# Kernel tuning notes

Hardware: AMD Instinct MI355X
Metric: run time of the kernel (lower is better)

The kernel has to match this reference:

```python
import jax, jax.numpy as jnp
import numpy as np

B, L, D = 1, 2048, 3072
NH, HD = 24, 128
MLP = 12288  # 4*D


def setup_inputs() -> dict:
    key = jax.random.key(0)
    ks = jax.random.split(key, 12)
    s = 0.02
    return {
        "scratchA": jnp.zeros((B, L, D + MLP), jnp.float32),
        "x": jax.random.normal(ks[0], (B, L, D), jnp.float32),
        "vec": jax.random.normal(ks[1], (B, D), jnp.float32),
        "pe": jax.random.normal(ks[2], (1, 1, L, HD // 2, 2, 2), jnp.float32),
        # Modulation: Linear(D, 3*D), stored as [in, out]
        "mod_w": jax.random.normal(ks[3], (D, 3 * D), jnp.float32) * s,
        "mod_b": jnp.zeros((3 * D,), jnp.float32),
        # linear1: Linear(D, 3*D + MLP)
        "w1": jax.random.normal(ks[4], (D, 3 * D + MLP), jnp.float32) * s,
        "b1": jnp.zeros((3 * D + MLP,), jnp.float32),
        # linear2: Linear(D + MLP, D)
        "w2": jax.random.normal(ks[5], (D + MLP, D), jnp.float32) * s,
        "b2": jnp.zeros((D,), jnp.float32),
        # QKNorm RMSNorm scales over head_dim
        "q_scale": jnp.ones((HD,), jnp.float32),
        "k_scale": jnp.ones((HD,), jnp.float32),
    }


def _rms_norm(t, scale, eps=1e-6):
    n = jax.lax.rsqrt(jnp.mean(t * t, axis=-1, keepdims=True) + eps)
    return t * (n * scale)


def _layer_norm(t, eps=1e-6):
    mu = jnp.mean(t, axis=-1, keepdims=True)
    var = jnp.mean(jnp.square(t - mu), axis=-1, keepdims=True)
    return (t - mu) * jax.lax.rsqrt(var + eps)


def _apply_rope(t, pe):
    # t: [B, NH, L, HD]; pe: [1, 1, L, HD//2, 2, 2]
    b, h, l, d = t.shape
    tr = t.reshape(b, h, l, d // 2, 1, 2)
    out = pe[..., 0] * tr[..., 0] + pe[..., 1] * tr[..., 1]  # [B,NH,L,HD//2,2]
    return out.reshape(b, h, l, d)


def reference(scratchA, x, vec, pe, mod_w, mod_b, w1, b1, w2, b2, q_scale, k_scale):
    # Modulation: silu + linear + chunk(3)
    mod = (jnp.dot(jax.nn.silu(vec), mod_w) + mod_b)[:, None, :]  # [B,1,3D]
    mod_shift, mod_scale, mod_gate = jnp.split(mod, 3, axis=-1)

    # adaLN modulation of pre-norm
    x_mod = mod_shift + (1.0 + mod_scale) * _layer_norm(x)

    # fused linear1 -> qkv + mlp
    h = jnp.dot(x_mod, w1) + b1  # [B, L, 3D + MLP]
    qkv, mlp = h[..., : 3 * D], h[..., 3 * D :]
    qkv = qkv.reshape(B, L, 3, NH, HD).transpose(2, 0, 3, 1, 4)  # [3,B,NH,L,HD]
    q, k, v = qkv[0], qkv[1], qkv[2]

    # QK RMSNorm
    q = _rms_norm(q, q_scale)
    k = _rms_norm(k, k_scale)

    # RoPE
    q = _apply_rope(q, pe)
    k = _apply_rope(k, pe)

    # scaled dot-product attention
    scale = HD ** -0.5
    scores = jnp.einsum("bhqd,bhkd->bhqk", q, k) * scale
    probs = jax.nn.softmax(scores, axis=-1)
    attn = jnp.einsum("bhqk,bhkd->bhqd", probs, v)  # [B,NH,L,HD]
    attn = attn.transpose(0, 2, 1, 3).reshape(B, L, D)

    # scratch buffer = [attention out | gelu(mlp)] (scratchA is just a buffer)
    scratch = jnp.concatenate([attn, jax.nn.gelu(mlp, approximate=True)], axis=-1)

    out = jnp.dot(scratch, w2) + b2
    return x + mod_gate * out
```

## Files before the change

kernel.cpp:

```cpp
#include <hip/hip_runtime.h>

typedef unsigned short u16;
typedef __bf16 bf16x8 __attribute__((ext_vector_type(8)));
typedef float f32x4 __attribute__((ext_vector_type(4)));

#define L_    2048
#define D_    3072
#define NH_   24
#define HD_   128
#define MLP_  12288
#define HCOLS 21504
#define SCOLS 15360

__device__ __forceinline__ float bf2f(u16 u) { return __uint_as_float(((unsigned)u) << 16); }
__device__ __forceinline__ u16 f2bf(float f) {
    unsigned b = __float_as_uint(f);
    b += 0x7FFF + ((b >> 16) & 1);
    return (u16)(b >> 16);
}
__device__ __forceinline__ void gld_lds16(const u16* g, u16* l) {
    __builtin_amdgcn_global_load_lds((const __attribute__((address_space(1))) void*)g,
                                     (__attribute__((address_space(3))) void*)l, 16, 0, 0);
}

template <int BM, int BN>
__global__ __launch_bounds__(256) void gemm_bt(
    const u16* __restrict__ A, const u16* __restrict__ Bt,
    const float* __restrict__ bias, void* __restrict__ Cv,
    int M, int N, int K, int ldC,
    long long sA, long long sB, long long sC,
    float alpha, int outBf16)
{
    constexpr int BK = 32;
    __shared__ __align__(16) u16 As[BM * BK];
    __shared__ __align__(16) u16 Bs[BN * BK];
    const int t = threadIdx.x, w = t >> 6, lane = t & 63;
    const int quad = lane >> 4, r16 = lane & 15;
    const int m0 = blockIdx.y * BM, n0 = blockIdx.x * BN;
    const u16* Ab = A + (size_t)blockIdx.z * sA;
    const u16* Bb = Bt + (size_t)blockIdx.z * sB;
    constexpr int WM = BM / 2, WN = BN / 2, TI = WM / 16, TJ = WN / 16;
    const int wm = (w >> 1) * WM, wn = (w & 1) * WN;

    f32x4 acc[TI][TJ];
#pragma unroll
    for (int i = 0; i < TI; ++i)
#pragma unroll
        for (int j = 0; j < TJ; ++j) acc[i][j] = (f32x4){0.f, 0.f, 0.f, 0.f};

    constexpr int AR = (BM * BK * 2) / 4096;
    constexpr int BR = (BN * BK * 2) / 4096;

    for (int k0 = 0; k0 < K; k0 += BK) {
#pragma unroll
        for (int r = 0; r < AR; ++r) {
            int o = r * 4096 + w * 1024 + lane * 16;
            int row = o >> 6, cb = o & 63;
            gld_lds16(Ab + (size_t)(m0 + row) * K + k0 + (cb >> 1), As + (o >> 1));
        }
#pragma unroll
        for (int r = 0; r < BR; ++r) {
            int o = r * 4096 + w * 1024 + lane * 16;
            int row = o >> 6, cb = o & 63;
            gld_lds16(Bb + (size_t)(n0 + row) * K + k0 + (cb >> 1), Bs + (o >> 1));
        }
        __syncthreads();
        bf16x8 af[TI], bfr[TJ];
#pragma unroll
        for (int i = 0; i < TI; ++i)
            af[i] = *(const bf16x8*)&As[(wm + i * 16 + r16) * BK + quad * 8];
#pragma unroll
        for (int j = 0; j < TJ; ++j)
            bfr[j] = *(const bf16x8*)&Bs[(wn + j * 16 + r16) * BK + quad * 8];
#pragma unroll
        for (int i = 0; i < TI; ++i)
#pragma unroll
            for (int j = 0; j < TJ; ++j)
                acc[i][j] = __builtin_amdgcn_mfma_f32_16x16x32_bf16(af[i], bfr[j], acc[i][j], 0, 0, 0);
        __syncthreads();
    }

    if (outBf16) {
        u16* Cb = (u16*)Cv + (size_t)blockIdx.z * sC;
#pragma unroll
        for (int i = 0; i < TI; ++i)
#pragma unroll
            for (int rr = 0; rr < 4; ++rr) {
                int m = m0 + wm + i * 16 + quad * 4 + rr;
                u16* crow = Cb + (size_t)m * ldC;
#pragma unroll
                for (int j = 0; j < TJ; ++j) {
                    int n = n0 + wn + j * 16 + r16;
                    float v = acc[i][j][rr] * alpha;
                    if (bias) v += bias[n];
                    crow[n] = f2bf(v);
                }
            }
    } else {
        float* Cb = (float*)Cv + (size_t)blockIdx.z * sC;
#pragma unroll
        for (int i = 0; i < TI; ++i)
#pragma unroll
            for (int rr = 0; rr < 4; ++rr) {
                int m = m0 + wm + i * 16 + quad * 4 + rr;
                float* crow = Cb + (size_t)m * ldC;
#pragma unroll
                for (int j = 0; j < TJ; ++j) {
                    int n = n0 + wn + j * 16 + r16;
                    float v = acc[i][j][rr] * alpha;
                    if (bias) v += bias[n];
                    crow[n] = v;
                }
            }
    }
}

__global__ __launch_bounds__(256) void transpose_to_bf16(
    const float* __restrict__ in, u16* __restrict__ out, int R, int C)
{
    __shared__ float tile[32][33];
    int c0 = blockIdx.x * 32, r0 = blockIdx.y * 32;
    int tx = threadIdx.x & 31, ty = threadIdx.x >> 5;
#pragma unroll
    for (int i = 0; i < 32; i += 8)
        tile[ty + i][tx] = in[(size_t)(r0 + ty + i) * C + c0 + tx];
    __syncthreads();
#pragma unroll
    for (int i = 0; i < 32; i += 8)
        out[(size_t)(c0 + ty + i) * R + r0 + tx] = f2bf(tile[tx][ty + i]);
}

__global__ void mod_init(const float* __restrict__ mod_b, const float* __restrict__ vec,
                         float* __restrict__ MOD, float* __restrict__ SVEC)
{
    int i = blockIdx.x * 256 + threadIdx.x;
    if (i < 3 * D_) MOD[i] = mod_b[i];
    if (i < D_) { float v = vec[i]; SVEC[i] = v / (1.f + __expf(-v)); }
}

__global__ __launch_bounds__(256) void mod_gemv(
    const float* __restrict__ SVEC, const float* __restrict__ mod_w, float* __restrict__ MOD)
{
    int n = blockIdx.x * 256 + threadIdx.x;
    int k0 = blockIdx.y * 128;
    float acc = 0.f;
#pragma unroll 8
    for (int kk = 0; kk < 128; ++kk)
        acc += SVEC[k0 + kk] * mod_w[(size_t)(k0 + kk) * (3 * D_) + n];
    atomicAdd(&MOD[n], acc);
}

__global__ __launch_bounds__(256) void ln_mod_k(
    const float* __restrict__ x, const float* __restrict__ MOD, u16* __restrict__ XMOD)
{
    int l = blockIdx.x, t = threadIdx.x;
    const float4* xr = (const float4*)(x + (size_t)l * D_);
    float4 v[3];
    float s = 0.f, ss = 0.f;
#pragma unroll
    for (int c = 0; c < 3; ++c) {
        v[c] = xr[c * 256 + t];
        s += v[c].x + v[c].y + v[c].z + v[c].w;
        ss += v[c].x * v[c].x + v[c].y * v[c].y + v[c].z * v[c].z + v[c].w * v[c].w;
    }
    __shared__ float rs[4], rss[4];
    float a = s, b = ss;
    for (int off = 32; off; off >>= 1) { a += __shfl_down(a, off); b += __shfl_down(b, off); }
    if ((t & 63) == 0) { rs[t >> 6] = a; rss[t >> 6] = b; }
    __syncthreads();
    float S = rs[0] + rs[1] + rs[2] + rs[3];
    float SS = rss[0] + rss[1] + rss[2] + rss[3];
    float mu = S * (1.f / D_);
    float var = SS * (1.f / D_) - mu * mu;
    float rstd = rsqrtf(var + 1e-6f);
    u16* orow = XMOD + (size_t)l * D_;
#pragma unroll
    for (int c = 0; c < 3; ++c) {
        int d0 = (c * 256 + t) * 4;
        float vals[4] = {v[c].x, v[c].y, v[c].z, v[c].w};
#pragma unroll
        for (int q = 0; q < 4; ++q) {
            int d = d0 + q;
            float o = MOD[d] + (1.f + MOD[D_ + d]) * ((vals[q] - mu) * rstd);
            orow[d] = f2bf(o);
        }
    }
}

__global__ __launch_bounds__(128) void qkv_rope(
    const u16* __restrict__ h, const float* __restrict__ pe,
    const float* __restrict__ qs, const float* __restrict__ ks,
    u16* __restrict__ Q, u16* __restrict__ Kb)
{
    int l = blockIdx.x, nh = blockIdx.y, tt = blockIdx.z;
    int d = threadIdx.x;
    float xv = bf2f(h[(size_t)l * HCOLS + tt * D_ + nh * HD_ + d]);
    __shared__ float red[2];
    __shared__ float ybuf[HD_];
    float sq = xv * xv;
    for (int off = 32; off; off >>= 1) sq += __shfl_down(sq, off);
    if ((d & 63) == 0) red[d >> 6] = sq;
    __syncthreads();
    float tot = red[0] + red[1];
    float rms = rsqrtf(tot * (1.f / HD_) + 1e-6f);
    const float* scale = (tt == 0) ? qs : ks;
    float y = xv * rms * scale[d];
    ybuf[d] = y;
    __syncthreads();
    int p = d >> 1, j = d & 1;
    float e = ybuf[2 * p], o = ybuf[2 * p + 1];
    const float* pb = pe + ((size_t)l * (HD_ / 2) + p) * 4 + j * 2;
    float out = pb[0] * e + pb[1] * o;
    u16* dst = (tt == 0) ? Q : Kb;
    dst[((size_t)nh * L_ + l) * HD_ + d] = f2bf(out);
}

__global__ __launch_bounds__(256) void v_trans(const u16* __restrict__ h, u16* __restrict__ VT)
{
    int lb = blockIdx.x, nh = blockIdx.y;
    __shared__ u16 tile[HD_][65];
    int t = threadIdx.x;
#pragma unroll
    for (int it = 0; it < 32; ++it) {
        int idx = it * 256 + t;
        int d = idx & 127, ll = idx >> 7;
        tile[d][ll] = h[(size_t)(lb * 64 + ll) * HCOLS + 2 * D_ + nh * HD_ + d];
    }
    __syncthreads();
#pragma unroll
    for (int it = 0; it < 32; ++it) {
        int idx = it * 256 + t;
        int ll = idx & 63, d = idx >> 6;
        VT[((size_t)nh * HD_ + d) * L_ + lb * 64 + ll] = tile[d][ll];
    }
}

__global__ __launch_bounds__(256) void gelu_k(const u16* __restrict__ h, u16* __restrict__ S)
{
    int l = blockIdx.y;
    int m = blockIdx.x * 256 + threadIdx.x;
    float v = bf2f(h[(size_t)l * HCOLS + 3 * D_ + m]);
    float c = 0.7978845608028654f * (v + 0.044715f * v * v * v);
    float g = 0.5f * v * (1.f + tanhf(c));
    S[(size_t)l * SCOLS + D_ + m] = f2bf(g);
}

__global__ __launch_bounds__(256) void softmax_k(const float* __restrict__ S, u16* __restrict__ P)
{
    const int t = threadIdx.x;
    const float* sr = S + (size_t)blockIdx.x * L_;
    u16* pr = P + (size_t)blockIdx.x * L_;
    float v[8];
    float mx = -3.4e38f;
#pragma unroll
    for (int c = 0; c < 8; ++c) { v[c] = sr[c * 256 + t]; mx = fmaxf(mx, v[c]); }
    __shared__ float red[4];
    for (int off = 32; off; off >>= 1) mx = fmaxf(mx, __shfl_down(mx, off));
    if ((t & 63) == 0) red[t >> 6] = mx;
    __syncthreads();
    mx = fmaxf(fmaxf(red[0], red[1]), fmaxf(red[2], red[3]));
    float sum = 0.f;
#pragma unroll
    for (int c = 0; c < 8; ++c) { v[c] = __expf(v[c] - mx); sum += v[c]; }
    __syncthreads();
    for (int off = 32; off; off >>= 1) sum += __shfl_down(sum, off);
    if ((t & 63) == 0) red[t >> 6] = sum;
    __syncthreads();
    sum = red[0] + red[1] + red[2] + red[3];
    float inv = 1.f / sum;
#pragma unroll
    for (int c = 0; c < 8; ++c) pr[c * 256 + t] = f2bf(v[c] * inv);
}

__global__ __launch_bounds__(256) void final_k(
    const float* __restrict__ x, const float* __restrict__ MOD,
    const float* __restrict__ G, float* __restrict__ out)
{
    int l = blockIdx.y;
    int d = blockIdx.x * 256 + threadIdx.x;
    size_t i = (size_t)l * D_ + d;
    out[i] = x[i] + MOD[2 * D_ + d] * G[i];
}

#define W1T_OFF   0ull
#define XMOD_OFF  132120576ull
#define W2T_OFF   144703488ull
#define Q_OFF     239075328ull
#define K_OFF     251658240ull
#define VT_OFF    264241152ull
#define SCR_OFF   276824064ull
#define MOD_OFF   339738624ull
#define SVEC_OFF  339775488ull
#define WS_NEED   339787776ull
#define SCORES_OFF 0ull
#define PROBS_OFF  67108864ull
#define G2_OFF     0ull

extern "C" void kernel_launch(void* const* d_in, const int* in_sizes, int n_in,
                              void* d_out, int out_size, void* d_ws, size_t ws_size,
                              hipStream_t stream)
{
    if (ws_size < WS_NEED) return;

    u16* hbuf = (u16*)d_in[0];
    const float* x     = (const float*)d_in[1];
    const float* vec   = (const float*)d_in[2];
    const float* pe    = (const float*)d_in[3];
    const float* mod_w = (const float*)d_in[4];
    const float* mod_b = (const float*)d_in[5];
    const float* w1    = (const float*)d_in[6];
    const float* b1    = (const float*)d_in[7];
    const float* w2    = (const float*)d_in[8];
    const float* b2    = (const float*)d_in[9];
    const float* qs    = (const float*)d_in[10];
    const float* ks    = (const float*)d_in[11];
    float* out = (float*)d_out;

    char* ws = (char*)d_ws;
    u16* W1T   = (u16*)(ws + W1T_OFF);
    u16* XMOD  = (u16*)(ws + XMOD_OFF);
    u16* W2T   = (u16*)(ws + W2T_OFF);
    u16* Qb    = (u16*)(ws + Q_OFF);
    u16* Kb    = (u16*)(ws + K_OFF);
    u16* VT    = (u16*)(ws + VT_OFF);
    u16* SCR   = (u16*)(ws + SCR_OFF);
    float* MOD  = (float*)(ws + MOD_OFF);
    float* SVEC = (float*)(ws + SVEC_OFF);
    float* SCORES = (float*)(ws + SCORES_OFF);
    u16* PROBS    = (u16*)(ws + PROBS_OFF);
    float* G2     = (float*)(ws + G2_OFF);

    transpose_to_bf16<<<dim3(HCOLS / 32, D_ / 32), 256, 0, stream>>>(w1, W1T, D_, HCOLS);
    transpose_to_bf16<<<dim3(D_ / 32, SCOLS / 32), 256, 0, stream>>>(w2, W2T, SCOLS, D_);

    mod_init<<<36, 256, 0, stream>>>(mod_b, vec, MOD, SVEC);
    mod_gemv<<<dim3(36, 24), 256, 0, stream>>>(SVEC, mod_w, MOD);

    ln_mod_k<<<L_, 256, 0, stream>>>(x, MOD, XMOD);

    gemm_bt<128, 128><<<dim3(HCOLS / 128, L_ / 128, 1), 256, 0, stream>>>(
        XMOD, W1T, b1, hbuf, L_, HCOLS, D_, HCOLS, 0, 0, 0, 1.f, 1);

    qkv_rope<<<dim3(L_, NH_, 2), 128, 0, stream>>>(hbuf, pe, qs, ks, Qb, Kb);
    v_trans<<<dim3(L_ / 64, NH_), 256, 0, stream>>>(hbuf, VT);
    gelu_k<<<dim3(MLP_ / 256, L_), 256, 0, stream>>>(hbuf, SCR);

    const float ascale = 0.08838834764831845f;
    for (int g = 0; g < 6; ++g) {
        const long long hoff = (long long)g * 4 * L_ * HD_;
        gemm_bt<128, 128><<<dim3(L_ / 128, L_ / 128, 4), 256, 0, stream>>>(
            Qb + hoff, Kb + hoff, nullptr, SCORES,
            L_, L_, HD_, L_, (long long)L_ * HD_, (long long)L_ * HD_, (long long)L_ * L_,
            ascale, 0);
        softmax_k<<<4 * L_, 256, 0, stream>>>(SCORES, PROBS);
        gemm_bt<64, 64><<<dim3(HD_ / 64, L_ / 64, 4), 256, 0, stream>>>(
            PROBS, VT + hoff, nullptr, SCR + (size_t)g * 4 * HD_,
            L_, HD_, L_, SCOLS, (long long)L_ * L_, (long long)HD_ * L_, HD_,
            1.f, 1);
    }

    gemm_bt<128, 128><<<dim3(D_ / 128, L_ / 128, 1), 256, 0, stream>>>(
        SCR, W2T, b2, G2, L_, D_, SCOLS, D_, 0, 0, 0, 1.f, 0);

    final_k<<<dim3(D_ / 256, L_), 256, 0, stream>>>(x, MOD, G2, out);
}
```

Baseline: 2.003 ms.

## Fuse GELU and residual gating into GEMM epilogues, swizzle LDS, bf16 scores

```diff
diff --git a/kernel.cpp b/kernel.cpp
--- a/kernel.cpp
+++ b/kernel.cpp
@@ -10,6 +10,7 @@
 #define HD_   128
 #define MLP_  12288
 #define HCOLS 21504
+#define QKVW  9216
 #define SCOLS 15360
 
 __device__ __forceinline__ float bf2f(u16 u) { return __uint_as_float(((unsigned)u) << 16); }
@@ -23,93 +24,100 @@
                                      (__attribute__((address_space(3))) void*)l, 16, 0, 0);
 }
 
-template <int BM, int BN>
-__global__ __launch_bounds__(256) void gemm_bt(
+template <int K, int LDC, int EPI>
+__global__ __launch_bounds__(256) void gemm128(
     const u16* __restrict__ A, const u16* __restrict__ Bt,
     const float* __restrict__ bias, void* __restrict__ Cv,
-    int M, int N, int K, int ldC,
-    long long sA, long long sB, long long sC,
-    float alpha, int outBf16)
+    long long sA, long long sB, long long sC, float alpha,
+    const float* __restrict__ resid, const float* __restrict__ gate)
 {
     constexpr int BK = 32;
-    __shared__ __align__(16) u16 As[BM * BK];
-    __shared__ __align__(16) u16 Bs[BN * BK];
+    __shared__ __align__(16) u16 As[128 * BK];
+    __shared__ __align__(16) u16 Bs[128 * BK];
     const int t = threadIdx.x, w = t >> 6, lane = t & 63;
     const int quad = lane >> 4, r16 = lane & 15;
-    const int m0 = blockIdx.y * BM, n0 = blockIdx.x * BN;
+    const int m0 = blockIdx.x * 128;
+    const int n0 = blockIdx.y * 128;
     const u16* Ab = A + (size_t)blockIdx.z * sA;
     const u16* Bb = Bt + (size_t)blockIdx.z * sB;
-    constexpr int WM = BM / 2, WN = BN / 2, TI = WM / 16, TJ = WN / 16;
-    const int wm = (w >> 1) * WM, wn = (w & 1) * WN;
-
-    f32x4 acc[TI][TJ];
-#pragma unroll
-    for (int i = 0; i < TI; ++i)
-#pragma unroll
-        for (int j = 0; j < TJ; ++j) acc[i][j] = (f32x4){0.f, 0.f, 0.f, 0.f};
-
-    constexpr int AR = (BM * BK * 2) / 4096;
-    constexpr int BR = (BN * BK * 2) / 4096;
+    const int wm = (w >> 1) * 64, wn = (w & 1) * 64;
+
+    f32x4 acc[4][4];
+#pragma unroll
+    for (int i = 0; i < 4; ++i)
+#pragma unroll
+        for (int j = 0; j < 4; ++j) acc[i][j] = (f32x4){0.f, 0.f, 0.f, 0.f};
 
     for (int k0 = 0; k0 < K; k0 += BK) {
 #pragma unroll
-        for (int r = 0; r < AR; ++r) {
+        for (int r = 0; r < 2; ++r) {
             int o = r * 4096 + w * 1024 + lane * 16;
-            int row = o >> 6, cb = o & 63;
-            gld_lds16(Ab + (size_t)(m0 + row) * K + k0 + (cb >> 1), As + (o >> 1));
-        }
-#pragma unroll
-        for (int r = 0; r < BR; ++r) {
+            int row = o >> 6, c = (o >> 4) & 3;
+            int gc = c ^ ((row >> 1) & 3);
+            gld_lds16(Ab + (size_t)(m0 + row) * K + k0 + gc * 8, As + (o >> 1));
+        }
+#pragma unroll
+        for (int r = 0; r < 2; ++r) {
             int o = r * 4096 + w * 1024 + lane * 16;
-            int row = o >> 6, cb = o & 63;
-            gld_lds16(Bb + (size_t)(n0 + row) * K + k0 + (cb >> 1), Bs + (o >> 1));
+            int row = o >> 6, c = (o >> 4) & 3;
+            int gc = c ^ ((row >> 1) & 3);
+            gld_lds16(Bb + (size_t)(n0 + row) * K + k0 + gc * 8, Bs + (o >> 1));
         }
         __syncthreads();
-        bf16x8 af[TI], bfr[TJ];
-#pragma unroll
-        for (int i = 0; i < TI; ++i)
-            af[i] = *(const bf16x8*)&As[(wm + i * 16 + r16) * BK + quad * 8];
-#pragma unroll
-        for (int j = 0; j < TJ; ++j)
-            bfr[j] = *(const bf16x8*)&Bs[(wn + j * 16 + r16) * BK + quad * 8];
-#pragma unroll
-        for (int i = 0; i < TI; ++i)
-#pragma unroll
-            for (int j = 0; j < TJ; ++j)
+        bf16x8 af[4], bfr[4];
+#pragma unroll
+        for (int i = 0; i < 4; ++i) {
+            int rA = wm + i * 16 + r16;
+            af[i] = *(const bf16x8*)&As[rA * 32 + ((quad ^ ((rA >> 1) & 3)) << 3)];
+        }
+#pragma unroll
+        for (int j = 0; j < 4; ++j) {
+            int rB = wn + j * 16 + r16;
+            bfr[j] = *(const bf16x8*)&Bs[rB * 32 + ((quad ^ ((rB >> 1) & 3)) << 3)];
+        }
+#pragma unroll
+        for (int i = 0; i < 4; ++i)
+#pragma unroll
+            for (int j = 0; j < 4; ++j)
                 acc[i][j] = __builtin_amdgcn_mfma_f32_16x16x32_bf16(af[i], bfr[j], acc[i][j], 0, 0, 0);
         __syncthreads();
     }
 
-    if (outBf16) {
-        u16* Cb = (u16*)Cv + (size_t)blockIdx.z * sC;
-#pragma unroll
-        for (int i = 0; i < TI; ++i)
+    if (EPI == 3) {
+        float* Cb = (float*)Cv + (size_t)blockIdx.z * sC;
+#pragma unroll
+        for (int i = 0; i < 4; ++i)
 #pragma unroll
             for (int rr = 0; rr < 4; ++rr) {
                 int m = m0 + wm + i * 16 + quad * 4 + rr;
-                u16* crow = Cb + (size_t)m * ldC;
-#pragma unroll
-                for (int j = 0; j < TJ; ++j) {
+                float* crow = Cb + (size_t)m * LDC;
+                const float* rrow = resid + (size_t)m * LDC;
+#pragma unroll
+                for (int j = 0; j < 4; ++j) {
                     int n = n0 + wn + j * 16 + r16;
                     float v = acc[i][j][rr] * alpha;
                     if (bias) v += bias[n];
-                    crow[n] = f2bf(v);
+                    crow[n] = rrow[n] + gate[n] * v;
                 }
             }
     } else {
-        float* Cb = (float*)Cv + (size_t)blockIdx.z * sC;
-#pragma unroll
-        for (int i = 0; i < TI; ++i)
+        u16* Cb = (u16*)Cv + (size_t)blockIdx.z * sC;
+#pragma unroll
+        for (int i = 0; i < 4; ++i)
 #pragma unroll
             for (int rr = 0; rr < 4; ++rr) {
                 int m = m0 + wm + i * 16 + quad * 4 + rr;
-                float* crow = Cb + (size_t)m * ldC;
-#pragma unroll
-                for (int j = 0; j < TJ; ++j) {
+                u16* crow = Cb + (size_t)m * LDC;
+#pragma unroll
+                for (int j = 0; j < 4; ++j) {
                     int n = n0 + wn + j * 16 + r16;
                     float v = acc[i][j][rr] * alpha;
                     if (bias) v += bias[n];
-                    crow[n] = v;
+                    if (EPI == 2) {
+                        float c = 0.7978845608028654f * (v + 0.044715f * v * v * v);
+                        v = v / (1.f + __expf(-2.f * c));
+                    }
+                    crow[n] = f2bf(v);
                 }
             }
     }
@@ -194,7 +202,7 @@
 {
     int l = blockIdx.x, nh = blockIdx.y, tt = blockIdx.z;
     int d = threadIdx.x;
-    float xv = bf2f(h[(size_t)l * HCOLS + tt * D_ + nh * HD_ + d]);
+    float xv = bf2f(h[(size_t)l * QKVW + tt * D_ + nh * HD_ + d]);
     __shared__ float red[2];
     __shared__ float ybuf[HD_];
     float sq = xv * xv;
@@ -224,7 +232,7 @@
     for (int it = 0; it < 32; ++it) {
         int idx = it * 256 + t;
         int d = idx & 127, ll = idx >> 7;
-        tile[d][ll] = h[(size_t)(lb * 64 + ll) * HCOLS + 2 * D_ + nh * HD_ + d];
+        tile[d][ll] = h[(size_t)(lb * 64 + ll) * QKVW + 2 * D_ + nh * HD_ + d];
     }
     __syncthreads();
 #pragma unroll
@@ -235,51 +243,42 @@
     }
 }
 
-__global__ __launch_bounds__(256) void gelu_k(const u16* __restrict__ h, u16* __restrict__ S)
-{
-    int l = blockIdx.y;
-    int m = blockIdx.x * 256 + threadIdx.x;
-    float v = bf2f(h[(size_t)l * HCOLS + 3 * D_ + m]);
-    float c = 0.7978845608028654f * (v + 0.044715f * v * v * v);
-    float g = 0.5f * v * (1.f + tanhf(c));
-    S[(size_t)l * SCOLS + D_ + m] = f2bf(g);
-}
-
-__global__ __launch_bounds__(256) void softmax_k(const float* __restrict__ S, u16* __restrict__ P)
+__global__ __launch_bounds__(256) void softmax_bf(u16* __restrict__ S)
 {
     const int t = threadIdx.x;
-    const float* sr = S + (size_t)blockIdx.x * L_;
-    u16* pr = P + (size_t)blockIdx.x * L_;
+    uint4* row = (uint4*)(S + (size_t)blockIdx.x * L_);
+    uint4 pk = row[t];
+    unsigned u[4] = {pk.x, pk.y, pk.z, pk.w};
     float v[8];
+#pragma unroll
+    for (int c = 0; c < 4; ++c) {
+        v[2 * c]     = bf2f((u16)(u[c] & 0xffff));
+        v[2 * c + 1] = bf2f((u16)(u[c] >> 16));
+    }
     float mx = -3.4e38f;
 #pragma unroll
-    for (int c = 0; c < 8; ++c) { v[c] = sr[c * 256 + t]; mx = fmaxf(mx, v[c]); }
+    for (int c = 0; c < 8; ++c) mx = fmaxf(mx, v[c]);
     __shared__ float red[4];
     for (int off = 32; off; off >>= 1) mx = fmaxf(mx, __shfl_down(mx, off));
     if ((t & 63) == 0) red[t >> 6] = mx;
     __syncthreads();
     mx = fmaxf(fmaxf(red[0], red[1]), fmaxf(red[2], red[3]));
-    float sum = 0.f;
-#pragma unroll
-    for (int c = 0; c < 8; ++c) { v[c] = __expf(v[c] - mx); sum += v[c]; }
-    __syncthreads();
-    for (int off = 32; off; off >>= 1) sum += __shfl_down(sum, off);
-    if ((t & 63) == 0) red[t >> 6] = sum;
-    __syncthreads();
-    sum = red[0] + red[1] + red[2] + red[3];
-    float inv = 1.f / sum;
-#pragma unroll
-    for (int c = 0; c < 8; ++c) pr[c * 256 + t] = f2bf(v[c] * inv);
-}
-
-__global__ __launch_bounds__(256) void final_k(
-    const float* __restrict__ x, const float* __restrict__ MOD,
-    const float* __restrict__ G, float* __restrict__ out)
-{
-    int l = blockIdx.y;
-    int d = blockIdx.x * 256 + threadIdx.x;
-    size_t i = (size_t)l * D_ + d;
-    out[i] = x[i] + MOD[2 * D_ + d] * G[i];
+    float s = 0.f;
+#pragma unroll
+    for (int c = 0; c < 8; ++c) { v[c] = __expf(v[c] - mx); s += v[c]; }
+    __syncthreads();
+    for (int off = 32; off; off >>= 1) s += __shfl_down(s, off);
+    if ((t & 63) == 0) red[t >> 6] = s;
+    __syncthreads();
+    s = red[0] + red[1] + red[2] + red[3];
+    float inv = 1.f / s;
+#pragma unroll
+    for (int c = 0; c < 4; ++c) {
+        unsigned lo = f2bf(v[2 * c] * inv);
+        unsigned hi = f2bf(v[2 * c + 1] * inv);
+        u[c] = lo | (hi << 16);
+    }
+    row[t] = make_uint4(u[0], u[1], u[2], u[3]);
 }
 
 #define W1T_OFF   0ull
@@ -292,9 +291,7 @@
 #define MOD_OFF   339738624ull
 #define SVEC_OFF  339775488ull
 #define WS_NEED   339787776ull
-#define SCORES_OFF 0ull
-#define PROBS_OFF  67108864ull
-#define G2_OFF     0ull
+#define PROBS_OFF 0ull
 
 extern "C" void kernel_launch(void* const* d_in, const int* in_sizes, int n_in,
                               void* d_out, int out_size, void* d_ws, size_t ws_size,
@@ -326,9 +323,7 @@
     u16* SCR   = (u16*)(ws + SCR_OFF);
     float* MOD  = (float*)(ws + MOD_OFF);
     float* SVEC = (float*)(ws + SVEC_OFF);
-    float* SCORES = (float*)(ws + SCORES_OFF);
-    u16* PROBS    = (u16*)(ws + PROBS_OFF);
-    float* G2     = (float*)(ws + G2_OFF);
+    u16* PROBS  = (u16*)(ws + PROBS_OFF);
 
     transpose_to_bf16<<<dim3(HCOLS / 32, D_ / 32), 256, 0, stream>>>(w1, W1T, D_, HCOLS);
     transpose_to_bf16<<<dim3(D_ / 32, SCOLS / 32), 256, 0, stream>>>(w2, W2T, SCOLS, D_);
@@ -338,29 +333,28 @@
 
     ln_mod_k<<<L_, 256, 0, stream>>>(x, MOD, XMOD);
 
-    gemm_bt<128, 128><<<dim3(HCOLS / 128, L_ / 128, 1), 256, 0, stream>>>(
-        XMOD, W1T, b1, hbuf, L_, HCOLS, D_, HCOLS, 0, 0, 0, 1.f, 1);
+    gemm128<3072, QKVW, 1><<<dim3(16, QKVW / 128, 1), 256, 0, stream>>>(
+        XMOD, W1T, b1, hbuf, 0, 0, 0, 1.f, nullptr, nullptr);
+    gemm128<3072, SCOLS, 2><<<dim3(16, MLP_ / 128, 1), 256, 0, stream>>>(
+        XMOD, W1T + (size_t)QKVW * 3072, b1 + QKVW, SCR + D_, 0, 0, 0, 1.f, nullptr, nullptr);
 
     qkv_rope<<<dim3(L_, NH_, 2), 128, 0, stream>>>(hbuf, pe, qs, ks, Qb, Kb);
     v_trans<<<dim3(L_ / 64, NH_), 256, 0, stream>>>(hbuf, VT);
-    gelu_k<<<dim3(MLP_ / 256, L_), 256, 0, stream>>>(hbuf, SCR);
 
     const float ascale = 0.08838834764831845f;
-    for (int g = 0; g < 6; ++g) {
-        const long long hoff = (long long)g * 4 * L_ * HD_;
-        gemm_bt<128, 128><<<dim3(L_ / 128, L_ / 128, 4), 256, 0, stream>>>(
-            Qb + hoff, Kb + hoff, nullptr, SCORES,
-            L_, L_, HD_, L_, (long long)L_ * HD_, (long long)L_ * HD_, (long long)L_ * L_,
-            ascale, 0);
-        softmax_k<<<4 * L_, 256, 0, stream>>>(SCORES, PROBS);
-        gemm_bt<64, 64><<<dim3(HD_ / 64, L_ / 64, 4), 256, 0, stream>>>(
-            PROBS, VT + hoff, nullptr, SCR + (size_t)g * 4 * HD_,
-            L_, HD_, L_, SCOLS, (long long)L_ * L_, (long long)HD_ * L_, HD_,
-            1.f, 1);
-    }
-
-    gemm_bt<128, 128><<<dim3(D_ / 128, L_ / 128, 1), 256, 0, stream>>>(
-        SCR, W2T, b2, G2, L_, D_, SCOLS, D_, 0, 0, 0, 1.f, 0);
-
-    final_k<<<dim3(D_ / 256, L_), 256, 0, stream>>>(x, MOD, G2, out);
-}
+    for (int g = 0; g < 2; ++g) {
+        const long long hoff = (long long)g * 12 * L_ * HD_;
+        gemm128<128, 2048, 1><<<dim3(16, 16, 12), 256, 0, stream>>>(
+            Qb + hoff, Kb + hoff, nullptr, PROBS,
+            (long long)L_ * HD_, (long long)L_ * HD_, (long long)L_ * L_,
+            ascale, nullptr, nullptr);
+        softmax_bf<<<12 * L_, 256, 0, stream>>>(PROBS);
+        gemm128<2048, SCOLS, 1><<<dim3(16, 1, 12), 256, 0, stream>>>(
+            PROBS, VT + hoff, nullptr, SCR + (size_t)g * 12 * HD_,
+            (long long)L_ * L_, (long long)HD_ * L_, (long long)HD_,
+            1.f, nullptr, nullptr);
+    }
+
+    gemm128<15360, D_, 3><<<dim3(16, D_ / 128, 1), 256, 0, stream>>>(
+        SCR, W2T, b2, out, 0, 0, 0, 1.f, x, MOD + 2 * D_);
+}
```

Result: faster. 1.719 ms (-14.2%).
